# Kernel optimization log

Hardware: AMD Instinct MI355X
Metric: run time of the kernel (lower is better)

Reference implementation:

```python
import jax, jax.numpy as jnp
import numpy as np
import math

B, S, D = 4096, 16, 256
HS, HT, O = 512, 512, 1


def setup_inputs() -> dict:
    key = jax.random.key(0)
    ks = jax.random.split(key, 20)
    stdv_s = 1.0 / math.sqrt(HS)
    stdv_t = 1.0 / math.sqrt(HT)
    u = lambda k, shape, s: jax.random.uniform(k, shape, jnp.float32, -s, s)
    return {
        "X": jax.random.normal(ks[0], (B, S, D), jnp.float32),
        # SpatialLSTM params (init uniform(-1/sqrt(H), 1/sqrt(H)) as in torch)
        "sa_W": u(ks[1], (D, 4 * HS), stdv_s),
        "sa_U": u(ks[2], (HS, 4 * HS), stdv_s),
        "sa_b": u(ks[3], (4 * HS,), stdv_s),
        "sa_Wa": u(ks[4], (D, D), stdv_s),
        "sa_Ua": u(ks[5], (2 * HS, D), stdv_s),
        "sa_ba": u(ks[6], (D,), stdv_s),
        "sa_Va": u(ks[7], (D, D), stdv_s),
        # TemporalLSTM params
        "ta_Wa": u(ks[8], (HS, S), stdv_t),
        "ta_Ua": u(ks[9], (HT, S), stdv_t),
        "ta_ba": u(ks[10], (S,), stdv_t),
        "ta_Va": u(ks[11], (S, S), stdv_t),
        "ta_W": u(ks[12], (HS, 4 * HT), stdv_t),
        "ta_U": u(ks[13], (HT, 4 * HT), stdv_t),
        "ta_b": u(ks[14], (4 * HT,), stdv_t),
        "ta_Wy": u(ks[15], (O, 4 * HT), stdv_t),
        "fc_W": u(ks[16], (O, HT), stdv_t),
        "fc_b": u(ks[17], (O,), stdv_t),
    }


def _lstm_update(gates, c, H):
    i = jax.nn.sigmoid(gates[:, :H])
    f = jax.nn.sigmoid(gates[:, H:2 * H])
    g = jnp.tanh(gates[:, 2 * H:3 * H])
    o = jax.nn.sigmoid(gates[:, 3 * H:])
    c_new = f * c + i * g
    h_new = o * jnp.tanh(c_new)
    return h_new, c_new


def _forward(X, sa_W, sa_U, sa_b, sa_Wa, sa_Ua, sa_ba, sa_Va,
             ta_Wa, ta_Ua, ta_ba, ta_Va, ta_W, ta_U, ta_b, ta_Wy, fc_W, fc_b):
    batch = X.shape[0]
    x = X  # x = X[:, :, 0:input_dim] == full X
    y0 = X[:, 0, D - 1:D]  # y = X[:, :, input_dim-1:], take t=0 -> [B, 1]

    # ---- Spatial attention LSTM over time ----
    def sa_step(carry, x_t):
        h, c = carry
        hc = jnp.concatenate([h, c], axis=1)  # [B, 2*HS]
        a_t = jnp.tanh(x_t @ sa_Wa + hc @ sa_Ua + sa_ba) @ sa_Va  # [B, D]
        alpha_t = jax.nn.softmax(a_t, axis=1)
        xt = alpha_t * x_t
        gates = xt @ sa_W + h @ sa_U + sa_b  # [B, 4*HS]
        h, c = _lstm_update(gates, c, HS)
        return (h, c), h

    h0 = jnp.zeros((batch, HS), X.dtype)
    c0 = jnp.zeros((batch, HS), X.dtype)
    _, hseq = jax.lax.scan(sa_step, (h0, c0), jnp.swapaxes(x, 0, 1))  # [S, B, HS]
    H3 = jnp.swapaxes(hseq, 0, 1)  # [B, S, HS]

    # ---- Temporal attention LSTM ----
    s0 = jnp.zeros((batch, HT), X.dtype)  # s_t is never updated in the original code

    def ta_step(carry, h_t):
        lh, lc, y_prev = carry
        beta = jnp.tanh(h_t @ ta_Wa + s0 @ ta_Ua + ta_ba) @ ta_Va  # [B, S]
        beta = jax.nn.softmax(beta, axis=1)
        h_ctx = jnp.einsum('bs,bsh->bh', beta, H3)  # [B, HS]
        gates = h_ctx @ ta_W + lh @ ta_U + y_prev @ ta_Wy + ta_b  # [B, 4*HT]
        lh, lc = _lstm_update(gates, lc, HT)
        y = lh @ fc_W.T + fc_b  # [B, O]
        return (lh, lc, y), None

    (_, _, y_pred), _ = jax.lax.scan(ta_step, (h0[:, :HT] * 0.0, c0[:, :HT] * 0.0, y0), hseq)
    return y_pred  # [B, O]


def reference(X, sa_W, sa_U, sa_b, sa_Wa, sa_Ua, sa_ba, sa_Va,
              ta_Wa, ta_Ua, ta_ba, ta_Va, ta_W, ta_U, ta_b, ta_Wy, fc_W, fc_b):
    return _forward(X, sa_W, sa_U, sa_b, sa_Wa, sa_Ua, sa_ba, sa_Va,
                    ta_Wa, ta_Ua, ta_ba, ta_Va, ta_W, ta_U, ta_b, ta_Wy, fc_W, fc_b)
```

## Files before the change

### kernel.cpp

```cpp
#include <hip/hip_runtime.h>


constexpr int Bb = 4096;
constexpr int Ss = 16;
constexpr int Dd = 256;
constexpr int Hh = 512;

typedef __attribute__((ext_vector_type(8))) short short8;
typedef __attribute__((ext_vector_type(4))) float f32x4;

__device__ __forceinline__ float sigm(float x) { return 1.0f / (1.0f + expf(-x)); }

__device__ __forceinline__ unsigned short f2bf(float x) {
    unsigned int u = __float_as_uint(x);
    u = (u + 0x7fffu + ((u >> 16) & 1u)) >> 16;
    return (unsigned short)u;
}
__device__ __forceinline__ float bf2f(unsigned short h) {
    return __uint_as_float(((unsigned int)h) << 16);
}
__device__ __forceinline__ void async16(const void* g, void* l) {
    __builtin_amdgcn_global_load_lds(
        (const __attribute__((address_space(1))) void*)g,
        (__attribute__((address_space(3))) void*)l, 16, 0, 0);
}
__device__ __forceinline__ short8 ldg8(const unsigned short* p) {
    return *reinterpret_cast<const short8*>(p);
}

struct SegB { const unsigned short* Ah; const unsigned short* Al;
              const unsigned short* Bh; const unsigned short* Bl;
              int lda; int ldb; int K; };

template<int BM, int BN, int NSEG, int EPI>
__global__ __launch_bounds__(256) void gemm_mfma_k(
    SegB s0, SegB s1, SegB s2,
    const float* __restrict__ bias,
    float* __restrict__ C,
    unsigned short* __restrict__ Th, unsigned short* __restrict__ Tl,
    int ldc)
{
    constexpr int WM = BM / 2, WN = BN / 2;
    constexpr int FI = WM / 16, FJ = WN / 16;
    __shared__ __align__(16) unsigned short sA[2][BM * 32];
    __shared__ __align__(16) unsigned short sB[2][BN * 32];
    const int tid  = threadIdx.x;
    const int lane = tid & 63;
    const int wv   = tid >> 6;
    const int wm   = wv & 1, wn = wv >> 1;
    const int row0 = blockIdx.x * BM;
    const int col0 = blockIdx.y * BN;

    f32x4 acc[FI][FJ];
#pragma unroll
    for (int i = 0; i < FI; i++)
#pragma unroll
        for (int j = 0; j < FJ; j++) acc[i][j] = (f32x4){0.f, 0.f, 0.f, 0.f};

    const int lrow = lane >> 2;
    const int lcol = (lane & 3) * 8;
    const int q8   = (lane >> 4) * 8;
    const int l15  = lane & 15;

#pragma unroll
    for (int sgi = 0; sgi < NSEG; ++sgi) {
        const SegB sg = (sgi == 0) ? s0 : ((sgi == 1) ? s1 : s2);
        const int K = sg.K;
        for (int k0 = 0; k0 < K; k0 += 32) {
#pragma unroll
            for (int c = wv; c < BM / 16; c += 4) {
                const int r = c * 16 + lrow;
                const size_t gA = (size_t)(row0 + r) * sg.lda + k0 + lcol;
                const int lo = c * 512 + lane * 8;
                async16(sg.Ah + gA, &sA[0][lo]);
                async16(sg.Al + gA, &sA[1][lo]);
            }
#pragma unroll
            for (int c = wv; c < BN / 16; c += 4) {
                const int r = c * 16 + lrow;
                const size_t gB = (size_t)(col0 + r) * sg.ldb + k0 + lcol;
                const int lo = c * 512 + lane * 8;
                async16(sg.Bh + gB, &sB[0][lo]);
                async16(sg.Bl + gB, &sB[1][lo]);
            }
            __syncthreads();
            short8 ah[FI], al[FI], bh[FJ], bl[FJ];
#pragma unroll
            for (int i = 0; i < FI; i++) {
                const int m = wm * WM + i * 16 + l15;
                ah[i] = *reinterpret_cast<const short8*>(&sA[0][m * 32 + q8]);
                al[i] = *reinterpret_cast<const short8*>(&sA[1][m * 32 + q8]);
            }
#pragma unroll
            for (int j = 0; j < FJ; j++) {
                const int n = wn * WN + j * 16 + l15;
                bh[j] = *reinterpret_cast<const short8*>(&sB[0][n * 32 + q8]);
                bl[j] = *reinterpret_cast<const short8*>(&sB[1][n * 32 + q8]);
            }
#pragma unroll
            for (int i = 0; i < FI; i++)
#pragma unroll
                for (int j = 0; j < FJ; j++) {
                    acc[i][j] = __builtin_amdgcn_mfma_f32_16x16x32_bf16(ah[i], bh[j], acc[i][j], 0, 0, 0);
                    acc[i][j] = __builtin_amdgcn_mfma_f32_16x16x32_bf16(ah[i], bl[j], acc[i][j], 0, 0, 0);
                    acc[i][j] = __builtin_amdgcn_mfma_f32_16x16x32_bf16(al[i], bh[j], acc[i][j], 0, 0, 0);
                }
            __syncthreads();
        }
    }
#pragma unroll
    for (int i = 0; i < FI; i++) {
#pragma unroll
        for (int j = 0; j < FJ; j++) {
            const int col = col0 + wn * WN + j * 16 + l15;
#pragma unroll
            for (int r = 0; r < 4; r++) {
                const int row = row0 + wm * WM + i * 16 + (lane >> 4) * 4 + r;
                float v = acc[i][j][r];
                if (EPI == 1) {
                    v = tanhf(v + bias[col]);
                    unsigned short hb = f2bf(v);
                    Th[(size_t)row * ldc + col] = hb;
                    Tl[(size_t)row * ldc + col] = f2bf(v - bf2f(hb));
                } else {
                    C[(size_t)row * ldc + col] = v;
                }
            }
        }
    }
}

template<int SPLITX>
__global__ __launch_bounds__(256) void a2sm_k(
    const unsigned short* __restrict__ tmph, const unsigned short* __restrict__ tmpl,
    const unsigned short* __restrict__ VaTh, const unsigned short* __restrict__ VaTl,
    const float* __restrict__ X, int t,
    unsigned short* __restrict__ xth, unsigned short* __restrict__ xtl,
    unsigned short* __restrict__ xsh, unsigned short* __restrict__ xsl)
{
    __shared__ __align__(16) unsigned short sB[2][256 * 32];
    __shared__ __align__(16) float av[16 * 260];
    __shared__ float rpart[16][16];
    __shared__ float spart[16][16];

    const int tid  = threadIdx.x;
    const int lane = tid & 63;
    const int wv   = tid >> 6;
    const int q8   = (lane >> 4) * 8;
    const int l15  = lane & 15;
    const int quad = lane >> 4;
    const int lrow = lane >> 2;
    const int lcol = (lane & 3) * 8;
    const int row0 = blockIdx.x * 16;

    short8 a_h[8], a_l[8];
#pragma unroll
    for (int kc = 0; kc < 8; kc++) {
        const size_t aoff = (size_t)(row0 + l15) * 256 + kc * 32 + q8;
        a_h[kc] = ldg8(tmph + aoff);
        a_l[kc] = ldg8(tmpl + aoff);
    }

    f32x4 acc[4];
#pragma unroll
    for (int j = 0; j < 4; j++) acc[j] = (f32x4){0.f, 0.f, 0.f, 0.f};

    for (int kc = 0; kc < 8; ++kc) {
        const int k0 = kc * 32;
#pragma unroll
        for (int c = wv; c < 16; c += 4) {
            const int n = c * 16 + lrow;
            const size_t gB = (size_t)n * 256 + k0 + lcol;
            const int lo = c * 512 + lane * 8;
            async16(VaTh + gB, &sB[0][lo]);
            async16(VaTl + gB, &sB[1][lo]);
        }
        __syncthreads();
#pragma unroll
        for (int j = 0; j < 4; j++) {
            const int n = wv * 64 + j * 16 + l15;
            const short8 b_h = *reinterpret_cast<const short8*>(&sB[0][n * 32 + q8]);
            const short8 b_l = *reinterpret_cast<const short8*>(&sB[1][n * 32 + q8]);
            acc[j] = __builtin_amdgcn_mfma_f32_16x16x32_bf16(a_h[kc], b_h, acc[j], 0, 0, 0);
            acc[j] = __builtin_amdgcn_mfma_f32_16x16x32_bf16(a_h[kc], b_l, acc[j], 0, 0, 0);
            acc[j] = __builtin_amdgcn_mfma_f32_16x16x32_bf16(a_l[kc], b_h, acc[j], 0, 0, 0);
        }
        __syncthreads();
    }

#pragma unroll
    for (int j = 0; j < 4; j++) {
        const int col = wv * 64 + j * 16 + l15;
#pragma unroll
        for (int r = 0; r < 4; r++) av[(quad * 4 + r) * 260 + col] = acc[j][r];
    }
    __syncthreads();

    const int row = tid >> 4;
    const int sl  = tid & 15;
    const int c0  = sl * 16;
    float* avr = av + row * 260;
    float mx = avr[c0];
#pragma unroll
    for (int i = 1; i < 16; i++) mx = fmaxf(mx, avr[c0 + i]);
    rpart[row][sl] = mx;
    __syncthreads();
    float M = rpart[row][0];
#pragma unroll
    for (int i = 1; i < 16; i++) M = fmaxf(M, rpart[row][i]);
    float s = 0.0f;
#pragma unroll
    for (int i = 0; i < 16; i++) {
        const float e = expf(avr[c0 + i] - M);
        avr[c0 + i] = e;
        s += e;
    }
    spart[row][sl] = s;
    __syncthreads();
    float S = spart[row][0];
#pragma unroll
    for (int i = 1; i < 16; i++) S += spart[row][i];
    const float inv = 1.0f / S;

    const size_t b = (size_t)(row0 + row);
    const float* Xr = X + b * (Ss * Dd) + (size_t)t * Dd + c0;
    unsigned short* xhp = xth + b * Dd + c0;
    unsigned short* xlp = xtl + b * Dd + c0;
#pragma unroll
    for (int g = 0; g < 4; g++) {
        const float4 xv = *reinterpret_cast<const float4*>(Xr + g * 4);
        const float v0 = avr[c0 + g * 4 + 0] * inv * xv.x;
        const float v1 = avr[c0 + g * 4 + 1] * inv * xv.y;
        const float v2 = avr[c0 + g * 4 + 2] * inv * xv.z;
        const float v3 = avr[c0 + g * 4 + 3] * inv * xv.w;
        ushort4 ho, lo;
        ho.x = f2bf(v0); lo.x = f2bf(v0 - bf2f(ho.x));
        ho.y = f2bf(v1); lo.y = f2bf(v1 - bf2f(ho.y));
        ho.z = f2bf(v2); lo.z = f2bf(v2 - bf2f(ho.z));
        ho.w = f2bf(v3); lo.w = f2bf(v3 - bf2f(ho.w));
        *reinterpret_cast<ushort4*>(xhp + g * 4) = ho;
        *reinterpret_cast<ushort4*>(xlp + g * 4) = lo;
    }
    if (SPLITX) {
        const float* Xn = X + b * (Ss * Dd) + (size_t)(t + 1) * Dd + c0;
        unsigned short* shp = xsh + b * Dd + c0;
        unsigned short* slp = xsl + b * Dd + c0;
#pragma unroll
        for (int g = 0; g < 4; g++) {
            const float4 xv = *reinterpret_cast<const float4*>(Xn + g * 4);
            ushort4 ho, lo;
            ho.x = f2bf(xv.x); lo.x = f2bf(xv.x - bf2f(ho.x));
            ho.y = f2bf(xv.y); lo.y = f2bf(xv.y - bf2f(ho.y));
            ho.z = f2bf(xv.z); lo.z = f2bf(xv.z - bf2f(ho.z));
            ho.w = f2bf(xv.w); lo.w = f2bf(xv.w - bf2f(ho.w));
            *reinterpret_cast<ushort4*>(shp + g * 4) = ho;
            *reinterpret_cast<ushort4*>(slp + g * 4) = lo;
        }
    }
}

template<int NSEG, int ZC, int TA>
__global__ __launch_bounds__(256) void gemm_gates_k(
    SegB s0, SegB s1,
    const float* __restrict__ bias,
    const float* __restrict__ wy,
    const float* __restrict__ yv,
    float* __restrict__ c_io,
    unsigned short* __restrict__ hh, unsigned short* __restrict__ hl,
    unsigned short* __restrict__ ch, unsigned short* __restrict__ cl)
{
    __shared__ __align__(16) unsigned short sA[2][128 * 32];
    __shared__ __align__(16) unsigned short sB[2][128 * 32];
    const int tid  = threadIdx.x;
    const int lane = tid & 63;
    const int wv   = tid >> 6;
    const int wm   = wv & 1, wn = wv >> 1;
    const int row0 = blockIdx.x * 128;
    const int by32 = blockIdx.y * 32;

    f32x4 acc[4][4];
#pragma unroll
    for (int i = 0; i < 4; i++)
#pragma unroll
        for (int g = 0; g < 4; g++) acc[i][g] = (f32x4){0.f, 0.f, 0.f, 0.f};

    const int lrow = lane >> 2;
    const int lcol = (lane & 3) * 8;
    const int q8   = (lane >> 4) * 8;
    const int l15  = lane & 15;

#pragma unroll
    for (int sgi = 0; sgi < NSEG; ++sgi) {
        const SegB sg = (sgi == 0) ? s0 : s1;
        const int K = sg.K;
        for (int k0 = 0; k0 < K; k0 += 32) {
#pragma unroll
            for (int c = wv; c < 8; c += 4) {
                const int r = c * 16 + lrow;
                const size_t gA = (size_t)(row0 + r) * sg.lda + k0 + lcol;
                const int lo = c * 512 + lane * 8;
                async16(sg.Ah + gA, &sA[0][lo]);
                async16(sg.Al + gA, &sA[1][lo]);
            }
#pragma unroll
            for (int cc = wv; cc < 8; cc += 4) {
                const int g  = cc >> 1;
                const int jj = (cc & 1) * 16 + lrow;
                const int rowg = g * 512 + by32 + jj;
                const size_t gB = (size_t)rowg * sg.ldb + k0 + lcol;
                const int lo = cc * 512 + lane * 8;
                async16(sg.Bh + gB, &sB[0][lo]);
                async16(sg.Bl + gB, &sB[1][lo]);
            }
            __syncthreads();
            short8 ah[4], al[4], bh[4], bl[4];
#pragma unroll
            for (int i = 0; i < 4; i++) {
                const int m = wm * 64 + i * 16 + l15;
                ah[i] = *reinterpret_cast<const short8*>(&sA[0][m * 32 + q8]);
                al[i] = *reinterpret_cast<const short8*>(&sA[1][m * 32 + q8]);
            }
#pragma unroll
            for (int g = 0; g < 4; g++) {
                const int n = g * 32 + wn * 16 + l15;
                bh[g] = *reinterpret_cast<const short8*>(&sB[0][n * 32 + q8]);
                bl[g] = *reinterpret_cast<const short8*>(&sB[1][n * 32 + q8]);
            }
#pragma unroll
            for (int i = 0; i < 4; i++)
#pragma unroll
                for (int g = 0; g < 4; g++) {
                    acc[i][g] = __builtin_amdgcn_mfma_f32_16x16x32_bf16(ah[i], bh[g], acc[i][g], 0, 0, 0);
                    acc[i][g] = __builtin_amdgcn_mfma_f32_16x16x32_bf16(ah[i], bl[g], acc[i][g], 0, 0, 0);
                    acc[i][g] = __builtin_amdgcn_mfma_f32_16x16x32_bf16(al[i], bh[g], acc[i][g], 0, 0, 0);
                }
            __syncthreads();
        }
    }
    const int j = by32 + wn * 16 + l15;
    const float b0 = bias[j],            b1 = bias[Hh + j];
    const float b2 = bias[2 * Hh + j],   b3 = bias[3 * Hh + j];
    float w0 = 0.f, w1 = 0.f, w2 = 0.f, w3 = 0.f;
    if (TA) { w0 = wy[j]; w1 = wy[Hh + j]; w2 = wy[2 * Hh + j]; w3 = wy[3 * Hh + j]; }
#pragma unroll
    for (int i = 0; i < 4; i++) {
        const int rbase = row0 + wm * 64 + i * 16 + (lane >> 4) * 4;
#pragma unroll
        for (int r = 0; r < 4; r++) {
            const int row = rbase + r;
            float gi = acc[i][0][r] + b0;
            float gf = acc[i][1][r] + b1;
            float gg = acc[i][2][r] + b2;
            float go = acc[i][3][r] + b3;
            if (TA) {
                const float yb = yv[row];
                gi += yb * w0; gf += yb * w1; gg += yb * w2; go += yb * w3;
            }
            const float i_ = sigm(gi), f_ = sigm(gf), gv = tanhf(gg), o_ = sigm(go);
            const size_t idx = (size_t)row * Hh + j;
            const float cp = ZC ? 0.0f : c_io[idx];
            const float c = f_ * cp + i_ * gv;
            c_io[idx] = c;
            const float h = o_ * tanhf(c);
            const unsigned short hb = f2bf(h);
            hh[idx] = hb;
            hl[idx] = f2bf(h - bf2f(hb));
            if (!TA) {
                const unsigned short cb = f2bf(c);
                ch[idx] = cb;
                cl[idx] = f2bf(c - bf2f(cb));
            }
        }
    }
}

__global__ __launch_bounds__(256) void splitT_k(const float* __restrict__ W,
                                                unsigned short* __restrict__ Th,
                                                unsigned short* __restrict__ Tl,
                                                int Kd, int Nd)
{
    __shared__ float tile[32][33];
    const int bk = blockIdx.x * 32, bn = blockIdx.y * 32;
    const int tid = threadIdx.x;
    const int r = tid >> 3, c4 = (tid & 7) * 4;
    const float4 v = *reinterpret_cast<const float4*>(&W[(size_t)(bk + r) * Nd + bn + c4]);
    tile[r][c4 + 0] = v.x; tile[r][c4 + 1] = v.y;
    tile[r][c4 + 2] = v.z; tile[r][c4 + 3] = v.w;
    __syncthreads();
    const int n = r, k4 = c4;
    ushort4 hq, lq;
    unsigned short* hp = (unsigned short*)&hq;
    unsigned short* lp = (unsigned short*)&lq;
#pragma unroll
    for (int q = 0; q < 4; q++) {
        float x = tile[k4 + q][n];
        unsigned short h = f2bf(x);
        hp[q] = h;
        lp[q] = f2bf(x - bf2f(h));
    }
    *reinterpret_cast<ushort4*>(&Th[(size_t)(bn + n) * Kd + bk + k4]) = hq;
    *reinterpret_cast<ushort4*>(&Tl[(size_t)(bn + n) * Kd + bk + k4]) = lq;
}

__global__ __launch_bounds__(256) void splitWa_k(const float* __restrict__ W,
                                                 unsigned short* __restrict__ Th,
                                                 unsigned short* __restrict__ Tl)
{
    int idx = blockIdx.x * 256 + threadIdx.x;
    int n = idx >> 9, k = idx & 511;
    float x = W[(size_t)k * 16 + n];
    unsigned short h = f2bf(x);
    Th[idx] = h;
    Tl[idx] = f2bf(x - bf2f(h));
}

__global__ __launch_bounds__(256) void init_k(const float* __restrict__ X,
                                              unsigned short* __restrict__ xsh,
                                              unsigned short* __restrict__ xsl,
                                              float* __restrict__ yv)
{
    int idx = blockIdx.x * 256 + threadIdx.x;
    int b = idx >> 8, d = idx & 255;
    float xv = X[(size_t)b * (Ss * Dd) + d];
    unsigned short hb = f2bf(xv);
    xsh[idx] = hb;
    xsl[idx] = f2bf(xv - bf2f(hb));
    if (d == Dd - 1) yv[b] = xv;
}

__global__ __launch_bounds__(256) void beta_k(const unsigned short* __restrict__ H3h,
                                              const unsigned short* __restrict__ H3l,
                                              const unsigned short* __restrict__ WaTh,
                                              const unsigned short* __restrict__ WaTl,
                                              const float* __restrict__ taba,
                                              const float* __restrict__ taVa,
                                              float* __restrict__ beta)
{
    __shared__ __align__(16) unsigned short sW[2][16 * 512];
    __shared__ __align__(16) unsigned short sA[2][128 * 32];
    __shared__ float tt[128][17];
    __shared__ float Vas[256];
    const int tid  = threadIdx.x;
    const int lane = tid & 63;
    const int wv   = tid >> 6;
    const int lrow = lane >> 2;
    const int lcol = (lane & 3) * 8;
    const int q8   = (lane >> 4) * 8;
    const int l15  = lane & 15;
    const size_t row0 = (size_t)blockIdx.x * 128;

#pragma unroll
    for (int it = 0; it < 4; ++it) {
        const int lo = wv * 2048 + it * 512 + lane * 8;
        async16(WaTh + lo, &sW[0][lo]);
        async16(WaTl + lo, &sW[1][lo]);
    }
    Vas[tid] = taVa[tid];

    f32x4 acc[2];
    acc[0] = (f32x4){0.f, 0.f, 0.f, 0.f};
    acc[1] = (f32x4){0.f, 0.f, 0.f, 0.f};

    for (int kc = 0; kc < 16; ++kc) {
        const int k0 = kc * 32;
#pragma unroll
        for (int c = wv; c < 8; c += 4) {
            const int r = c * 16 + lrow;
            const size_t gA = (row0 + r) * Hh + k0 + lcol;
            const int lo = c * 512 + lane * 8;
            async16(H3h + gA, &sA[0][lo]);
            async16(H3l + gA, &sA[1][lo]);
        }
        __syncthreads();
        const short8 bh = *reinterpret_cast<const short8*>(&sW[0][l15 * 512 + k0 + q8]);
        const short8 bl = *reinterpret_cast<const short8*>(&sW[1][l15 * 512 + k0 + q8]);
#pragma unroll
        for (int i = 0; i < 2; i++) {
            const int m = wv * 32 + i * 16 + l15;
            const short8 ah = *reinterpret_cast<const short8*>(&sA[0][m * 32 + q8]);
            const short8 al = *reinterpret_cast<const short8*>(&sA[1][m * 32 + q8]);
            acc[i] = __builtin_amdgcn_mfma_f32_16x16x32_bf16(ah, bh, acc[i], 0, 0, 0);
            acc[i] = __builtin_amdgcn_mfma_f32_16x16x32_bf16(ah, bl, acc[i], 0, 0, 0);
            acc[i] = __builtin_amdgcn_mfma_f32_16x16x32_bf16(al, bh, acc[i], 0, 0, 0);
        }
        __syncthreads();
    }
    const float ba = taba[l15];
#pragma unroll
    for (int i = 0; i < 2; i++) {
#pragma unroll
        for (int r = 0; r < 4; r++) {
            const int rl = wv * 32 + i * 16 + (lane >> 4) * 4 + r;
            tt[rl][l15] = tanhf(acc[i][r] + ba);
        }
    }
    __syncthreads();
    if (tid < 128) {
        float tv[16];
#pragma unroll
        for (int m = 0; m < 16; m++) tv[m] = tt[tid][m];
        float l[16];
        float mx = -1e30f;
#pragma unroll
        for (int n = 0; n < 16; n++) {
            float s = 0.0f;
#pragma unroll
            for (int m = 0; m < 16; m++) s = fmaf(tv[m], Vas[m * 16 + n], s);
            l[n] = s;
            mx = fmaxf(mx, s);
        }
        float sum = 0.0f;
#pragma unroll
        for (int n = 0; n < 16; n++) { l[n] = expf(l[n] - mx); sum += l[n]; }
        const float inv = 1.0f / sum;
        float* bp = beta + (row0 + tid) * 16;
#pragma unroll
        for (int n4 = 0; n4 < 4; n4++) {
            float4 v = { l[n4 * 4] * inv, l[n4 * 4 + 1] * inv,
                         l[n4 * 4 + 2] * inv, l[n4 * 4 + 3] * inv };
            *reinterpret_cast<float4*>(bp + n4 * 4) = v;
        }
    }
}

__global__ __launch_bounds__(256) void hctx_all_k(unsigned short* __restrict__ H3h,
                                                  unsigned short* __restrict__ H3l,
                                                  const float* __restrict__ beta)
{
    const int b = blockIdx.x, tid = threadIdx.x;
    __shared__ float bs[16][16];
    {
        const int t = tid >> 4, s = tid & 15;
        bs[t][s] = beta[((size_t)t * Bb + b) * 16 + s];
    }
    float h0[16], h1[16];
    const int e0 = tid * 2;
#pragma unroll
    for (int s = 0; s < 16; s++) {
        const size_t o = ((size_t)s * Bb + b) * Hh + e0;
        const ushort2 hv = *reinterpret_cast<const ushort2*>(&H3h[o]);
        const ushort2 lv = *reinterpret_cast<const ushort2*>(&H3l[o]);
        h0[s] = bf2f(hv.x) + bf2f(lv.x);
        h1[s] = bf2f(hv.y) + bf2f(lv.y);
    }
    __syncthreads();
#pragma unroll
    for (int t = 0; t < 16; t++) {
        float a0 = 0.f, a1 = 0.f;
#pragma unroll
        for (int s = 0; s < 16; s++) {
            const float w = bs[t][s];
            a0 = fmaf(w, h0[s], a0);
            a1 = fmaf(w, h1[s], a1);
        }
        ushort2 ho, lo;
        ho.x = f2bf(a0); lo.x = f2bf(a0 - bf2f(ho.x));
        ho.y = f2bf(a1); lo.y = f2bf(a1 - bf2f(ho.y));
        const size_t o = ((size_t)t * Bb + b) * Hh + e0;
        *reinterpret_cast<ushort2*>(&H3h[o]) = ho;
        *reinterpret_cast<ushort2*>(&H3l[o]) = lo;
    }
}

__global__ __launch_bounds__(256) void y_k(const unsigned short* __restrict__ hh,
                                           const unsigned short* __restrict__ hl,
                                           const float* __restrict__ fcW,
                                           const float* __restrict__ fcb,
                                           float* __restrict__ yv,
                                           float* __restrict__ outp)
{
    int b = blockIdx.x, tid = threadIdx.x;
    size_t o = (size_t)b * Hh + tid;
    float h0 = bf2f(hh[o]) + bf2f(hl[o]);
    float h1 = bf2f(hh[o + 256]) + bf2f(hl[o + 256]);
    float p = h0 * fcW[tid] + h1 * fcW[tid + 256];
#pragma unroll
    for (int off = 32; off > 0; off >>= 1) p += __shfl_down(p, off, 64);
    __shared__ float wred[4];
    if ((tid & 63) == 0) wred[tid >> 6] = p;
    __syncthreads();
    if (tid == 0) {
        float y = fcb[0] + wred[0] + wred[1] + wred[2] + wred[3];
        yv[b] = y;
        if (outp) outp[b] = y;
    }
}

extern "C" void kernel_launch(void* const* d_in, const int* in_sizes, int n_in,
                              void* d_out, int out_size, void* d_ws, size_t ws_size,
                              hipStream_t stream)
{
    (void)in_sizes; (void)n_in; (void)out_size; (void)ws_size;
    const float* X     = (const float*)d_in[0];
    const float* sa_W  = (const float*)d_in[1];
    const float* sa_U  = (const float*)d_in[2];
    const float* sa_b  = (const float*)d_in[3];
    const float* sa_Wa = (const float*)d_in[4];
    const float* sa_Ua = (const float*)d_in[5];
    const float* sa_ba = (const float*)d_in[6];
    const float* sa_Va = (const float*)d_in[7];
    const float* ta_Wa = (const float*)d_in[8];
    const float* ta_ba = (const float*)d_in[10];
    const float* ta_Va = (const float*)d_in[11];
    const float* ta_W  = (const float*)d_in[12];
    const float* ta_U  = (const float*)d_in[13];
    const float* ta_b  = (const float*)d_in[14];
    const float* ta_Wy = (const float*)d_in[15];
    const float* fc_W  = (const float*)d_in[16];
    const float* fc_b  = (const float*)d_in[17];

    char* base = (char*)d_ws;
    size_t off = 0;
    auto alloc = [&](size_t bytes) {
        void* p = base + off; off += (bytes + 255) & ~(size_t)255; return p;
    };
    const size_t BH = (size_t)Bb * Hh;
    unsigned short* H3h = (unsigned short*)alloc((size_t)Ss * BH * 2);
    unsigned short* H3l = (unsigned short*)alloc((size_t)Ss * BH * 2);
    float* cbuf = (float*)alloc(BH * 4);
    float* lc   = (float*)alloc(BH * 4);
    unsigned short* lhBh = (unsigned short*)alloc(BH * 2);
    unsigned short* lhBl = (unsigned short*)alloc(BH * 2);
    unsigned short* xth = (unsigned short*)alloc((size_t)Bb * Dd * 2);
    unsigned short* xtl = (unsigned short*)alloc((size_t)Bb * Dd * 2);
    unsigned short* xsh = (unsigned short*)alloc((size_t)Bb * Dd * 2);
    unsigned short* xsl = (unsigned short*)alloc((size_t)Bb * Dd * 2);
    unsigned short* ch  = (unsigned short*)alloc(BH * 2);
    unsigned short* cl  = (unsigned short*)alloc(BH * 2);
    unsigned short* tmph = (unsigned short*)alloc((size_t)Bb * Dd * 2);
    unsigned short* tmpl = (unsigned short*)alloc((size_t)Bb * Dd * 2);
    unsigned short* saWth = (unsigned short*)alloc((size_t)Dd * 4 * Hh * 2);
    unsigned short* saWtl = (unsigned short*)alloc((size_t)Dd * 4 * Hh * 2);
    unsigned short* saUth = (unsigned short*)alloc((size_t)Hh * 4 * Hh * 2);
    unsigned short* saUtl = (unsigned short*)alloc((size_t)Hh * 4 * Hh * 2);
    unsigned short* taWth = (unsigned short*)alloc((size_t)Hh * 4 * Hh * 2);
    unsigned short* taWtl = (unsigned short*)alloc((size_t)Hh * 4 * Hh * 2);
    unsigned short* taUth = (unsigned short*)alloc((size_t)Hh * 4 * Hh * 2);
    unsigned short* taUtl = (unsigned short*)alloc((size_t)Hh * 4 * Hh * 2);
    unsigned short* WaTh = (unsigned short*)alloc((size_t)Dd * Dd * 2);
    unsigned short* WaTl = (unsigned short*)alloc((size_t)Dd * Dd * 2);
    unsigned short* UaTh = (unsigned short*)alloc((size_t)2 * Hh * Dd * 2);
    unsigned short* UaTl = (unsigned short*)alloc((size_t)2 * Hh * Dd * 2);
    unsigned short* VaTh = (unsigned short*)alloc((size_t)Dd * Dd * 2);
    unsigned short* VaTl = (unsigned short*)alloc((size_t)Dd * Dd * 2);
    unsigned short* tWaTh = (unsigned short*)alloc((size_t)16 * Hh * 2);
    unsigned short* tWaTl = (unsigned short*)alloc((size_t)16 * Hh * 2);
    float* yv = (float*)alloc((size_t)Bb * 4);
    float* beta = (float*)xth;
    unsigned short* lhAh = (unsigned short*)cbuf;
    unsigned short* lhAl = (unsigned short*)cbuf + BH;
    unsigned short* lhh[2] = { lhAh, lhBh };
    unsigned short* lhl[2] = { lhAl, lhBl };

    splitT_k<<<dim3(Dd / 32, (4 * Hh) / 32), 256, 0, stream>>>(sa_W, saWth, saWtl, Dd, 4 * Hh);
    splitT_k<<<dim3(Hh / 32, (4 * Hh) / 32), 256, 0, stream>>>(sa_U, saUth, saUtl, Hh, 4 * Hh);
    splitT_k<<<dim3(Hh / 32, (4 * Hh) / 32), 256, 0, stream>>>(ta_W, taWth, taWtl, Hh, 4 * Hh);
    splitT_k<<<dim3(Hh / 32, (4 * Hh) / 32), 256, 0, stream>>>(ta_U, taUth, taUtl, Hh, 4 * Hh);
    splitT_k<<<dim3(Dd / 32, Dd / 32), 256, 0, stream>>>(sa_Wa, WaTh, WaTl, Dd, Dd);
    splitT_k<<<dim3((2 * Hh) / 32, Dd / 32), 256, 0, stream>>>(sa_Ua, UaTh, UaTl, 2 * Hh, Dd);
    splitT_k<<<dim3(Dd / 32, Dd / 32), 256, 0, stream>>>(sa_Va, VaTh, VaTl, Dd, Dd);
    splitWa_k<<<dim3(32), 256, 0, stream>>>(ta_Wa, tWaTh, tWaTl);
    init_k<<<dim3((Bb * Dd) / 256), 256, 0, stream>>>(X, xsh, xsl, yv);

    const dim3 agrid(Bb / 32, Dd / 32);
    const dim3 smgrid(Bb / 16);
    const dim3 ggrid(Bb / 128, Hh / 32);

    for (int t = 0; t < Ss; ++t) {
        SegB a0{ xsh, xsl, WaTh, WaTl, Dd, Dd, Dd };
        if (t == 0) {
            gemm_mfma_k<32, 32, 1, 1><<<agrid, 256, 0, stream>>>(
                a0, a0, a0, sa_ba, nullptr, tmph, tmpl, Dd);
        } else {
            SegB a1{ H3h + (size_t)(t - 1) * BH, H3l + (size_t)(t - 1) * BH,
                     UaTh, UaTl, Hh, 2 * Hh, Hh };
            SegB a2{ ch, cl, UaTh + Hh, UaTl + Hh, Hh, 2 * Hh, Hh };
            gemm_mfma_k<32, 32, 3, 1><<<agrid, 256, 0, stream>>>(
                a0, a1, a2, sa_ba, nullptr, tmph, tmpl, Dd);
        }

        if (t < Ss - 1)
            a2sm_k<1><<<smgrid, 256, 0, stream>>>(
                tmph, tmpl, VaTh, VaTl, X, t, xth, xtl, xsh, xsl);
        else
            a2sm_k<0><<<smgrid, 256, 0, stream>>>(
                tmph, tmpl, VaTh, VaTl, X, t, xth, xtl, xsh, xsl);

        SegB g0{ xth, xtl, saWth, saWtl, Dd, Dd, Dd };
        if (t == 0) {
            gemm_gates_k<1, 1, 0><<<ggrid, 256, 0, stream>>>(
                g0, g0, sa_b, nullptr, nullptr, cbuf,
                H3h + (size_t)t * BH, H3l + (size_t)t * BH, ch, cl);
        } else {
            SegB g1{ H3h + (size_t)(t - 1) * BH, H3l + (size_t)(t - 1) * BH,
                     saUth, saUtl, Hh, Hh, Hh };
            gemm_gates_k<2, 0, 0><<<ggrid, 256, 0, stream>>>(
                g0, g1, sa_b, nullptr, nullptr, cbuf,
                H3h + (size_t)t * BH, H3l + (size_t)t * BH, ch, cl);
        }
    }

    beta_k<<<dim3((Ss * Bb) / 128), 256, 0, stream>>>(
        H3h, H3l, tWaTh, tWaTl, ta_ba, ta_Va, beta);
    hctx_all_k<<<dim3(Bb), 256, 0, stream>>>(H3h, H3l, beta);

    for (int t = 0; t < Ss; ++t) {
        SegB g0{ H3h + (size_t)t * BH, H3l + (size_t)t * BH,
                 taWth, taWtl, Hh, Hh, Hh };
        const int po = t & 1;
        if (t == 0) {
            gemm_gates_k<1, 1, 1><<<ggrid, 256, 0, stream>>>(
                g0, g0, ta_b, ta_Wy, yv, lc, lhh[0], lhl[0], nullptr, nullptr);
        } else {
            SegB g1{ lhh[(t - 1) & 1], lhl[(t - 1) & 1], taUth, taUtl, Hh, Hh, Hh };
            gemm_gates_k<2, 0, 1><<<ggrid, 256, 0, stream>>>(
                g0, g1, ta_b, ta_Wy, yv, lc, lhh[po], lhl[po], nullptr, nullptr);
        }
        y_k<<<Bb, 256, 0, stream>>>(lhh[po], lhl[po], fc_W, fc_b, yv,
                                    (t == Ss - 1) ? (float*)d_out : nullptr);
    }
}
```

Baseline: 2.396 ms.

## Fuse fc output projection into gates epilogue and XOR-swizzle LDS tiles

Drops the separate per-step y_k kernel by computing the fc_W dot product inside the temporal gates GEMM epilogue, using a 16-lane shuffle reduction and an atomicAdd into a per-step y buffer that is pre-initialised with the bias. It also applies an XOR swizzle to the LDS column placement of the A and B tiles to reduce bank conflicts on the MFMA operand reads. This removes 16 kernel launches and re-reading h from global memory. In exchange, the atomics add contention and make summation order nondeterministic. The fused dot product also uses fp32 h directly instead of the bf16 hi/lo reconstruction.

```diff
diff --git a/kernel.cpp b/kernel.cpp
--- a/kernel.cpp
+++ b/kernel.cpp
@@ -265,6 +265,8 @@
     const float* __restrict__ bias,
     const float* __restrict__ wy,
     const float* __restrict__ yv,
+    const float* __restrict__ fcW,
+    float* __restrict__ yv_next,
     float* __restrict__ c_io,
     unsigned short* __restrict__ hh, unsigned short* __restrict__ hl,
     unsigned short* __restrict__ ch, unsigned short* __restrict__ cl)
@@ -284,10 +286,10 @@
 #pragma unroll
         for (int g = 0; g < 4; g++) acc[i][g] = (f32x4){0.f, 0.f, 0.f, 0.f};
 
-    const int lrow = lane >> 2;
-    const int lcol = (lane & 3) * 8;
-    const int q8   = (lane >> 4) * 8;
-    const int l15  = lane & 15;
+    const int lrow  = lane >> 2;
+    const int lcols = (((lane & 3) ^ ((lane >> 2) & 3)) * 8);
+    const int q8s   = (((lane >> 4) ^ (lane & 3)) * 8);
+    const int l15   = lane & 15;
 
 #pragma unroll
     for (int sgi = 0; sgi < NSEG; ++sgi) {
@@ -297,7 +299,7 @@
 #pragma unroll
             for (int c = wv; c < 8; c += 4) {
                 const int r = c * 16 + lrow;
-                const size_t gA = (size_t)(row0 + r) * sg.lda + k0 + lcol;
+                const size_t gA = (size_t)(row0 + r) * sg.lda + k0 + lcols;
                 const int lo = c * 512 + lane * 8;
                 async16(sg.Ah + gA, &sA[0][lo]);
                 async16(sg.Al + gA, &sA[1][lo]);
@@ -307,7 +309,7 @@
                 const int g  = cc >> 1;
                 const int jj = (cc & 1) * 16 + lrow;
                 const int rowg = g * 512 + by32 + jj;
-                const size_t gB = (size_t)rowg * sg.ldb + k0 + lcol;
+                const size_t gB = (size_t)rowg * sg.ldb + k0 + lcols;
                 const int lo = cc * 512 + lane * 8;
                 async16(sg.Bh + gB, &sB[0][lo]);
                 async16(sg.Bl + gB, &sB[1][lo]);
@@ -317,14 +319,14 @@
 #pragma unroll
             for (int i = 0; i < 4; i++) {
                 const int m = wm * 64 + i * 16 + l15;
-                ah[i] = *reinterpret_cast<const short8*>(&sA[0][m * 32 + q8]);
-                al[i] = *reinterpret_cast<const short8*>(&sA[1][m * 32 + q8]);
+                ah[i] = *reinterpret_cast<const short8*>(&sA[0][m * 32 + q8s]);
+                al[i] = *reinterpret_cast<const short8*>(&sA[1][m * 32 + q8s]);
             }
 #pragma unroll
             for (int g = 0; g < 4; g++) {
                 const int n = g * 32 + wn * 16 + l15;
-                bh[g] = *reinterpret_cast<const short8*>(&sB[0][n * 32 + q8]);
-                bl[g] = *reinterpret_cast<const short8*>(&sB[1][n * 32 + q8]);
+                bh[g] = *reinterpret_cast<const short8*>(&sB[0][n * 32 + q8s]);
+                bl[g] = *reinterpret_cast<const short8*>(&sB[1][n * 32 + q8s]);
             }
 #pragma unroll
             for (int i = 0; i < 4; i++)
@@ -340,8 +342,11 @@
     const int j = by32 + wn * 16 + l15;
     const float b0 = bias[j],            b1 = bias[Hh + j];
     const float b2 = bias[2 * Hh + j],   b3 = bias[3 * Hh + j];
-    float w0 = 0.f, w1 = 0.f, w2 = 0.f, w3 = 0.f;
-    if (TA) { w0 = wy[j]; w1 = wy[Hh + j]; w2 = wy[2 * Hh + j]; w3 = wy[3 * Hh + j]; }
+    float w0 = 0.f, w1 = 0.f, w2 = 0.f, w3 = 0.f, fw = 0.f;
+    if (TA) {
+        w0 = wy[j]; w1 = wy[Hh + j]; w2 = wy[2 * Hh + j]; w3 = wy[3 * Hh + j];
+        fw = fcW[j];
+    }
 #pragma unroll
     for (int i = 0; i < 4; i++) {
         const int rbase = row0 + wm * 64 + i * 16 + (lane >> 4) * 4;
@@ -369,6 +374,13 @@
                 const unsigned short cb = f2bf(c);
                 ch[idx] = cb;
                 cl[idx] = f2bf(c - bf2f(cb));
+            } else {
+                float p = h * fw;
+                p += __shfl_xor(p, 1, 64);
+                p += __shfl_xor(p, 2, 64);
+                p += __shfl_xor(p, 4, 64);
+                p += __shfl_xor(p, 8, 64);
+                if (l15 == 0) atomicAdd(&yv_next[row], p);
             }
         }
     }
@@ -428,6 +440,20 @@
     if (d == Dd - 1) yv[b] = xv;
 }
 
+__global__ __launch_bounds__(256) void yinit_k(const float* __restrict__ fcb,
+                                               float* __restrict__ yvs)
+{
+    int idx = blockIdx.x * 256 + threadIdx.x;
+    yvs[idx] = fcb[0];
+}
+
+__global__ __launch_bounds__(256) void yout_k(const float* __restrict__ ylast,
+                                              float* __restrict__ outp)
+{
+    int idx = blockIdx.x * 256 + threadIdx.x;
+    outp[idx] = ylast[idx];
+}
+
 __global__ __launch_bounds__(256) void beta_k(const unsigned short* __restrict__ H3h,
                                               const unsigned short* __restrict__ H3l,
                                               const unsigned short* __restrict__ WaTh,
@@ -559,30 +585,6 @@
         const size_t o = ((size_t)t * Bb + b) * Hh + e0;
         *reinterpret_cast<ushort2*>(&H3h[o]) = ho;
         *reinterpret_cast<ushort2*>(&H3l[o]) = lo;
-    }
-}
-
-__global__ __launch_bounds__(256) void y_k(const unsigned short* __restrict__ hh,
-                                           const unsigned short* __restrict__ hl,
-                                           const float* __restrict__ fcW,
-                                           const float* __restrict__ fcb,
-                                           float* __restrict__ yv,
-                                           float* __restrict__ outp)
-{
-    int b = blockIdx.x, tid = threadIdx.x;
-    size_t o = (size_t)b * Hh + tid;
-    float h0 = bf2f(hh[o]) + bf2f(hl[o]);
-    float h1 = bf2f(hh[o + 256]) + bf2f(hl[o + 256]);
-    float p = h0 * fcW[tid] + h1 * fcW[tid + 256];
-#pragma unroll
-    for (int off = 32; off > 0; off >>= 1) p += __shfl_down(p, off, 64);
-    __shared__ float wred[4];
-    if ((tid & 63) == 0) wred[tid >> 6] = p;
-    __syncthreads();
-    if (tid == 0) {
-        float y = fcb[0] + wred[0] + wred[1] + wred[2] + wred[3];
-        yv[b] = y;
-        if (outp) outp[b] = y;
     }
 }
 
@@ -645,7 +647,8 @@
     unsigned short* VaTl = (unsigned short*)alloc((size_t)Dd * Dd * 2);
     unsigned short* tWaTh = (unsigned short*)alloc((size_t)16 * Hh * 2);
     unsigned short* tWaTl = (unsigned short*)alloc((size_t)16 * Hh * 2);
-    float* yv = (float*)alloc((size_t)Bb * 4);
+    float* yv  = (float*)alloc((size_t)Bb * 4);
+    float* yvs = (float*)alloc((size_t)Ss * Bb * 4);
     float* beta = (float*)xth;
     unsigned short* lhAh = (unsigned short*)cbuf;
     unsigned short* lhAl = (unsigned short*)cbuf + BH;
@@ -661,6 +664,7 @@
     splitT_k<<<dim3(Dd / 32, Dd / 32), 256, 0, stream>>>(sa_Va, VaTh, VaTl, Dd, Dd);
     splitWa_k<<<dim3(32), 256, 0, stream>>>(ta_Wa, tWaTh, tWaTl);
     init_k<<<dim3((Bb * Dd) / 256), 256, 0, stream>>>(X, xsh, xsl, yv);
+    yinit_k<<<dim3((Ss * Bb) / 256), 256, 0, stream>>>(fc_b, yvs);
 
     const dim3 agrid(Bb / 32, Dd / 32);
     const dim3 smgrid(Bb / 16);
@@ -689,13 +693,13 @@
         SegB g0{ xth, xtl, saWth, saWtl, Dd, Dd, Dd };
         if (t == 0) {
             gemm_gates_k<1, 1, 0><<<ggrid, 256, 0, stream>>>(
-                g0, g0, sa_b, nullptr, nullptr, cbuf,
+                g0, g0, sa_b, nullptr, nullptr, nullptr, nullptr, cbuf,
                 H3h + (size_t)t * BH, H3l + (size_t)t * BH, ch, cl);
         } else {
             SegB g1{ H3h + (size_t)(t - 1) * BH, H3l + (size_t)(t - 1) * BH,
                      saUth, saUtl, Hh, Hh, Hh };
             gemm_gates_k<2, 0, 0><<<ggrid, 256, 0, stream>>>(
-                g0, g1, sa_b, nullptr, nullptr, cbuf,
+                g0, g1, sa_b, nullptr, nullptr, nullptr, nullptr, cbuf,
                 H3h + (size_t)t * BH, H3l + (size_t)t * BH, ch, cl);
         }
     }
@@ -708,15 +712,19 @@
         SegB g0{ H3h + (size_t)t * BH, H3l + (size_t)t * BH,
                  taWth, taWtl, Hh, Hh, Hh };
         const int po = t & 1;
+        const float* yprev = (t == 0) ? yv : (yvs + (size_t)(t - 1) * Bb);
+        float* ynext = yvs + (size_t)t * Bb;
         if (t == 0) {
             gemm_gates_k<1, 1, 1><<<ggrid, 256, 0, stream>>>(
-                g0, g0, ta_b, ta_Wy, yv, lc, lhh[0], lhl[0], nullptr, nullptr);
+                g0, g0, ta_b, ta_Wy, yprev, fc_W, ynext, lc,
+                lhh[0], lhl[0], nullptr, nullptr);
         } else {
             SegB g1{ lhh[(t - 1) & 1], lhl[(t - 1) & 1], taUth, taUtl, Hh, Hh, Hh };
             gemm_gates_k<2, 0, 1><<<ggrid, 256, 0, stream>>>(
-                g0, g1, ta_b, ta_Wy, yv, lc, lhh[po], lhl[po], nullptr, nullptr);
-        }
-        y_k<<<Bb, 256, 0, stream>>>(lhh[po], lhl[po], fc_W, fc_b, yv,
-                                    (t == Ss - 1) ? (float*)d_out : nullptr);
-    }
-}
+                g0, g1, ta_b, ta_Wy, yprev, fc_W, ynext, lc,
+                lhh[po], lhl[po], nullptr, nullptr);
+        }
+    }
+    yout_k<<<dim3(Bb / 256), 256, 0, stream>>>(yvs + (size_t)(Ss - 1) * Bb,
+                                               (float*)d_out);
+}
```

After: 2.450 ms. 1.02x slower.

## Fuse temporal y projection into gates GEMM and drop per-step y kernel

Applied to the files above, without the earlier changes.

Computes the previous step's output y = lh·fc_W + fc_b inside the temporal gates GEMM. It reuses the lh A-fragments already staged in shared memory for the U segment and adds extra MFMAs with a split-bf16 copy of fc_W. This removes 15 separate y_k launches and the global round trip of y between steps, leaving one y_k after the loop. In exchange, every block in the grid redundantly computes y for its rows, which adds MFMA work and registers to the gates kernel.

```diff
diff --git a/kernel.cpp b/kernel.cpp
--- a/kernel.cpp
+++ b/kernel.cpp
@@ -265,6 +265,9 @@
     const float* __restrict__ bias,
     const float* __restrict__ wy,
     const float* __restrict__ yv,
+    const float* __restrict__ fcb,
+    const unsigned short* __restrict__ fswh,
+    const unsigned short* __restrict__ fswl,
     float* __restrict__ c_io,
     unsigned short* __restrict__ hh, unsigned short* __restrict__ hl,
     unsigned short* __restrict__ ch, unsigned short* __restrict__ cl)
@@ -283,6 +286,9 @@
     for (int i = 0; i < 4; i++)
 #pragma unroll
         for (int g = 0; g < 4; g++) acc[i][g] = (f32x4){0.f, 0.f, 0.f, 0.f};
+    f32x4 yacc[4];
+#pragma unroll
+    for (int i = 0; i < 4; i++) yacc[i] = (f32x4){0.f, 0.f, 0.f, 0.f};
 
     const int lrow = lane >> 2;
     const int lcol = (lane & 3) * 8;
@@ -334,14 +340,27 @@
                     acc[i][g] = __builtin_amdgcn_mfma_f32_16x16x32_bf16(ah[i], bl[g], acc[i][g], 0, 0, 0);
                     acc[i][g] = __builtin_amdgcn_mfma_f32_16x16x32_bf16(al[i], bh[g], acc[i][g], 0, 0, 0);
                 }
+            if (TA && NSEG == 2 && sgi == 1) {
+                const short8 fwh = ldg8(fswh + k0 + q8);
+                const short8 fwl = ldg8(fswl + k0 + q8);
+#pragma unroll
+                for (int i = 0; i < 4; i++) {
+                    yacc[i] = __builtin_amdgcn_mfma_f32_16x16x32_bf16(ah[i], fwh, yacc[i], 0, 0, 0);
+                    yacc[i] = __builtin_amdgcn_mfma_f32_16x16x32_bf16(ah[i], fwl, yacc[i], 0, 0, 0);
+                    yacc[i] = __builtin_amdgcn_mfma_f32_16x16x32_bf16(al[i], fwh, yacc[i], 0, 0, 0);
+                }
+            }
             __syncthreads();
         }
     }
     const int j = by32 + wn * 16 + l15;
     const float b0 = bias[j],            b1 = bias[Hh + j];
     const float b2 = bias[2 * Hh + j],   b3 = bias[3 * Hh + j];
-    float w0 = 0.f, w1 = 0.f, w2 = 0.f, w3 = 0.f;
-    if (TA) { w0 = wy[j]; w1 = wy[Hh + j]; w2 = wy[2 * Hh + j]; w3 = wy[3 * Hh + j]; }
+    float w0 = 0.f, w1 = 0.f, w2 = 0.f, w3 = 0.f, fb = 0.f;
+    if (TA) {
+        w0 = wy[j]; w1 = wy[Hh + j]; w2 = wy[2 * Hh + j]; w3 = wy[3 * Hh + j];
+        fb = fcb[0];
+    }
 #pragma unroll
     for (int i = 0; i < 4; i++) {
         const int rbase = row0 + wm * 64 + i * 16 + (lane >> 4) * 4;
@@ -353,7 +372,7 @@
             float gg = acc[i][2][r] + b2;
             float go = acc[i][3][r] + b3;
             if (TA) {
-                const float yb = yv[row];
+                const float yb = (NSEG == 1) ? yv[row] : (yacc[i][r] + fb);
                 gi += yb * w0; gf += yb * w1; gg += yb * w2; go += yb * w3;
             }
             const float i_ = sigm(gi), f_ = sigm(gf), gv = tanhf(gg), o_ = sigm(go);
@@ -409,6 +428,17 @@
     int idx = blockIdx.x * 256 + threadIdx.x;
     int n = idx >> 9, k = idx & 511;
     float x = W[(size_t)k * 16 + n];
+    unsigned short h = f2bf(x);
+    Th[idx] = h;
+    Tl[idx] = f2bf(x - bf2f(h));
+}
+
+__global__ __launch_bounds__(256) void splitFc_k(const float* __restrict__ W,
+                                                 unsigned short* __restrict__ Th,
+                                                 unsigned short* __restrict__ Tl)
+{
+    int idx = blockIdx.x * 256 + threadIdx.x;
+    float x = W[idx];
     unsigned short h = f2bf(x);
     Th[idx] = h;
     Tl[idx] = f2bf(x - bf2f(h));
@@ -645,6 +675,8 @@
     unsigned short* VaTl = (unsigned short*)alloc((size_t)Dd * Dd * 2);
     unsigned short* tWaTh = (unsigned short*)alloc((size_t)16 * Hh * 2);
     unsigned short* tWaTl = (unsigned short*)alloc((size_t)16 * Hh * 2);
+    unsigned short* fswh = (unsigned short*)alloc((size_t)Hh * 2);
+    unsigned short* fswl = (unsigned short*)alloc((size_t)Hh * 2);
     float* yv = (float*)alloc((size_t)Bb * 4);
     float* beta = (float*)xth;
     unsigned short* lhAh = (unsigned short*)cbuf;
@@ -660,6 +692,7 @@
     splitT_k<<<dim3((2 * Hh) / 32, Dd / 32), 256, 0, stream>>>(sa_Ua, UaTh, UaTl, 2 * Hh, Dd);
     splitT_k<<<dim3(Dd / 32, Dd / 32), 256, 0, stream>>>(sa_Va, VaTh, VaTl, Dd, Dd);
     splitWa_k<<<dim3(32), 256, 0, stream>>>(ta_Wa, tWaTh, tWaTl);
+    splitFc_k<<<dim3(2), 256, 0, stream>>>(fc_W, fswh, fswl);
     init_k<<<dim3((Bb * Dd) / 256), 256, 0, stream>>>(X, xsh, xsl, yv);
 
     const dim3 agrid(Bb / 32, Dd / 32);
@@ -689,13 +722,13 @@
         SegB g0{ xth, xtl, saWth, saWtl, Dd, Dd, Dd };
         if (t == 0) {
             gemm_gates_k<1, 1, 0><<<ggrid, 256, 0, stream>>>(
-                g0, g0, sa_b, nullptr, nullptr, cbuf,
+                g0, g0, sa_b, nullptr, nullptr, nullptr, nullptr, nullptr, cbuf,
                 H3h + (size_t)t * BH, H3l + (size_t)t * BH, ch, cl);
         } else {
             SegB g1{ H3h + (size_t)(t - 1) * BH, H3l + (size_t)(t - 1) * BH,
                      saUth, saUtl, Hh, Hh, Hh };
             gemm_gates_k<2, 0, 0><<<ggrid, 256, 0, stream>>>(
-                g0, g1, sa_b, nullptr, nullptr, cbuf,
+                g0, g1, sa_b, nullptr, nullptr, nullptr, nullptr, nullptr, cbuf,
                 H3h + (size_t)t * BH, H3l + (size_t)t * BH, ch, cl);
         }
     }
@@ -710,13 +743,14 @@
         const int po = t & 1;
         if (t == 0) {
             gemm_gates_k<1, 1, 1><<<ggrid, 256, 0, stream>>>(
-                g0, g0, ta_b, ta_Wy, yv, lc, lhh[0], lhl[0], nullptr, nullptr);
+                g0, g0, ta_b, ta_Wy, yv, fc_b, fswh, fswl, lc,
+                lhh[0], lhl[0], nullptr, nullptr);
         } else {
             SegB g1{ lhh[(t - 1) & 1], lhl[(t - 1) & 1], taUth, taUtl, Hh, Hh, Hh };
             gemm_gates_k<2, 0, 1><<<ggrid, 256, 0, stream>>>(
-                g0, g1, ta_b, ta_Wy, yv, lc, lhh[po], lhl[po], nullptr, nullptr);
-        }
-        y_k<<<Bb, 256, 0, stream>>>(lhh[po], lhl[po], fc_W, fc_b, yv,
-                                    (t == Ss - 1) ? (float*)d_out : nullptr);
-    }
-}
+                g0, g1, ta_b, ta_Wy, yv, fc_b, fswh, fswl, lc,
+                lhh[po], lhl[po], nullptr, nullptr);
+        }
+    }
+    y_k<<<dim3(Bb), 256, 0, stream>>>(lhh[1], lhl[1], fc_W, fc_b, yv, (float*)d_out);
+}
```

New measurement: 2.425 ms. Within noise of the previous version (+1.2%).
